# Performance work log

Hardware: AMD Instinct MI355X
Metric: run time of the kernel (lower is better)

The kernel has to match this reference:

```python
import jax, jax.numpy as jnp
import numpy as np

N, C, H, O = 100000, 128, 256, 1
T, K = 8192, 32
NHEAD, DH, FF = 8, 16, 512
NEG = -1e9

def _ln(x, g, b):
    mu = x.mean(-1, keepdims=True)
    v = x.var(-1, keepdims=True)
    return (x - mu) / jnp.sqrt(v + 1e-5) * g + b


def setup_inputs() -> dict:
    key = jax.random.key(0)
    ks = jax.random.split(key, 40)
    w = lambda k, s: jax.random.normal(k, s, jnp.float32) * 0.02
    inp = {
        'x': jax.random.normal(ks[0], (N, C), jnp.float32),
        'tar_ei': jax.random.randint(ks[1], (2, T), 0, N),
        'cn_cols': jax.random.randint(ks[2], (T, K), 0, N),
        'cn_counts': jax.random.randint(ks[3], (T,), 0, K + 1),
        'beta': jnp.ones((1,), jnp.float32),
        # cn_tokenlin: Linear(4C -> C) + ReLU
        'tok_w': w(ks[4], (C, 4 * C)), 'tok_b': w(ks[5], (C,)),
        # transformer encoder layer (norm_first, nhead=8, ff=512, gelu)
        'ln1_g': jnp.ones((C,), jnp.float32), 'ln1_b': jnp.zeros((C,), jnp.float32),
        'qkv_w': w(ks[6], (3 * C, C)), 'qkv_b': w(ks[7], (3 * C,)),
        'out_w': w(ks[8], (C, C)), 'out_b': w(ks[9], (C,)),
        'ln2_g': jnp.ones((C,), jnp.float32), 'ln2_b': jnp.zeros((C,), jnp.float32),
        'ff1_w': w(ks[10], (FF, C)), 'ff1_b': w(ks[11], (FF,)),
        'ff2_w': w(ks[12], (C, FF)), 'ff2_b': w(ks[13], (C,)),
        # xcnlin: Linear(C,H) ReLU Linear(H,H) ReLU Linear(H,H)
        'xcn_w1': w(ks[14], (H, C)), 'xcn_b1': w(ks[15], (H,)),
        'xcn_w2': w(ks[16], (H, H)), 'xcn_b2': w(ks[17], (H,)),
        'xcn_w3': w(ks[18], (H, H)), 'xcn_b3': w(ks[19], (H,)),
        # xijlin: Linear(C,H) ReLU Linear(H,H)
        'xij_w1': w(ks[20], (H, C)), 'xij_b1': w(ks[21], (H,)),
        'xij_w2': w(ks[22], (H, H)), 'xij_b2': w(ks[23], (H,)),
        # lin: Linear(H,H) ReLU Linear(H,O)
        'lin_w1': w(ks[24], (H, H)), 'lin_b1': w(ks[25], (H,)),
        'lin_w2': w(ks[26], (O, H)), 'lin_b2': w(ks[27], (O,)),
    }
    return inp


def _forward(x, beta, tok_w, tok_b, ln1_g, ln1_b, qkv_w, qkv_b, out_w, out_b,
             ln2_g, ln2_b, ff1_w, ff1_b, ff2_w, ff2_b,
             xcn_w1, xcn_b1, xcn_w2, xcn_b2, xcn_w3, xcn_b3,
             xij_w1, xij_b1, xij_w2, xij_b2, lin_w1, lin_b1, lin_w2, lin_b2,
             tar_ei, cn_cols, cn_counts):
    xi = x[tar_ei[0]]              # [T,C]
    xj = x[tar_ei[1]]              # [T,C]
    mask = jnp.arange(K)[None, :] < cn_counts[:, None]   # [T,K] valid token mask

    # --- per-(edge, common-neighbor) token features -----------------------
    xw = x[cn_cols]                # [T,K,C] gather of CN node features
    bc = lambda a: jnp.broadcast_to(a[:, None, :], (T, K, C))
    pf = jnp.concatenate([xw, bc(xi), bc(xj), bc(xi * xj)], axis=-1)  # [T,K,4C]
    tok = jax.nn.relu(pf @ tok_w.T + tok_b)               # [T,K,C]

    # --- pre-norm transformer encoder layer over the CN tokens ------------
    h = _ln(tok, ln1_g, ln1_b)
    qkv = h @ qkv_w.T + qkv_b
    q, k, v = jnp.split(qkv, 3, axis=-1)
    q = q.reshape(T, K, NHEAD, DH)
    k = k.reshape(T, K, NHEAD, DH)
    v = v.reshape(T, K, NHEAD, DH)
    scores = jnp.einsum('tqhd,tkhd->thqk', q, k) / jnp.sqrt(jnp.float32(DH))
    scores = jnp.where(mask[:, None, None, :], scores, NEG)  # key_padding_mask
    attn = jax.nn.softmax(scores, axis=-1)
    ctx = jnp.einsum('thqk,tkhd->tqhd', attn, v).reshape(T, K, C)
    tok = tok + ctx @ out_w.T + out_b
    h2 = _ln(tok, ln2_g, ln2_b)
    tok = tok + jax.nn.gelu(h2 @ ff1_w.T + ff1_b, approximate=False) @ ff2_w.T + ff2_b

    # mask out padding, mean-pool over valid CN tokens ----------------------
    tok = jnp.where(mask[..., None], tok, 0.0)
    denom = jnp.clip(cn_counts, 1)[:, None].astype(tok.dtype)
    xcn = tok.sum(axis=1) / denom                           # [T,C]; zero rows for 0 CNs

    # --- edge MLPs ---------------------------------------------------------
    hc = jax.nn.relu(xcn @ xcn_w1.T + xcn_b1)
    hc = jax.nn.relu(hc @ xcn_w2.T + xcn_b2)
    hc = hc @ xcn_w3.T + xcn_b3                              # xcnlin(xcn)
    xij = jax.nn.relu((xi * xj) @ xij_w1.T + xij_b1)
    xij = xij @ xij_w2.T + xij_b2                            # xijlin(xi*xj)
    z = jax.nn.relu((hc * beta + xij) @ lin_w1.T + lin_b1)
    return z @ lin_w2.T + lin_b2                             # [T,O]


def reference(x, tar_ei, cn_cols, cn_counts, beta, tok_w, tok_b, ln1_g, ln1_b,
              qkv_w, qkv_b, out_w, out_b, ln2_g, ln2_b, ff1_w, ff1_b, ff2_w, ff2_b,
              xcn_w1, xcn_b1, xcn_w2, xcn_b2, xcn_w3, xcn_b3,
              xij_w1, xij_b1, xij_w2, xij_b2, lin_w1, lin_b1, lin_w2, lin_b2):
    return _forward(x, beta, tok_w, tok_b, ln1_g, ln1_b, qkv_w, qkv_b, out_w, out_b,
                    ln2_g, ln2_b, ff1_w, ff1_b, ff2_w, ff2_b,
                    xcn_w1, xcn_b1, xcn_w2, xcn_b2, xcn_w3, xcn_b3,
                    xij_w1, xij_b1, xij_w2, xij_b2, lin_w1, lin_b1, lin_w2, lin_b2,
                    tar_ei, cn_cols, cn_counts)
```

## Files before the change

kernel.cpp:

```cpp
#include <hip/hip_runtime.h>
#include <hip/hip_bf16.h>
#include <math.h>

#define DI __device__ __forceinline__

typedef float  f32x4 __attribute__((ext_vector_type(4)));
typedef short  bf8   __attribute__((ext_vector_type(8)));
typedef unsigned short u16;

static constexpr int TT = 8192;
static constexpr int KK = 32;
static constexpr int CC = 128;

DI u16 f2bf(float x){ union{float f; unsigned u;} v; v.f = x; unsigned r = v.u + 0x7FFFu + ((v.u>>16)&1u); return (u16)(r>>16); }
DI float bf2f(u16 b){ union{unsigned u; float f;} v; v.u = ((unsigned)b)<<16; return v.f; }
DI unsigned pk2(float a, float b){ return (unsigned)f2bf(a) | ((unsigned)f2bf(b)<<16); }
DI f32x4 mfma16(bf8 a, bf8 b, f32x4 c){ return __builtin_amdgcn_mfma_f32_16x16x32_bf16(a, b, c, 0, 0, 0); }
DI int soff(int r, int c, int stride, int mask){ return r*stride + ((c*2) ^ ((r&mask)<<4)); }

struct WP { const float* p[12]; };

__global__ void k0_convert(WP wp, u16* __restrict__ dst){
  const int KS[11]  = {512,128,128,128,512,128,256,256,128,256,256};
  const int SH[11]  = {4,2,2,2,4,2,3,3,2,3,3};
  const int OFF[12] = {0,65536,114688,131072,196608,262144,294912,360448,425984,458752,524288,589824};
  int gid = blockIdx.x*256 + threadIdx.x;
  if (gid >= 590080) return;
  if (gid >= 589824){ dst[gid] = f2bf(wp.p[11][gid - 589824]); return; }
  #pragma unroll
  for (int s = 0; s < 11; s++){
    if (gid < OFF[s+1]){
      int i = gid - OFF[s];
      int e = i & 7, l = (i >> 3) & 63, t = i >> 9;
      int k32 = t & ((1 << SH[s]) - 1), n16 = t >> SH[s];
      int row = n16*16 + (l & 15);
      int col = k32*32 + ((l >> 4) << 3) + e;
      dst[gid] = f2bf(wp.p[s][row*KS[s] + col]);
      return;
    }
  }
}

#define O_TOK 0
#define O_H   16384
#define O_RG  32768
#define LDS_K1 53248

DI void layernorm64(const char* src, char* dst, const float* __restrict__ g,
                    const float* __restrict__ bta, int tid){
  int r = tid >> 2, q = tid & 3;
  float v[32]; float s = 0.f, sq = 0.f;
  #pragma unroll
  for (int i = 0; i < 4; i++){
    bf8 h8 = *(const bf8*)(src + soff(r, q*32 + i*8, 256, 7));
    #pragma unroll
    for (int j = 0; j < 8; j++){ float f = bf2f((u16)h8[j]); v[i*8+j] = f; s += f; sq += f*f; }
  }
  s  += __shfl_xor(s, 1);  s  += __shfl_xor(s, 2);
  sq += __shfl_xor(sq, 1); sq += __shfl_xor(sq, 2);
  float mu = s * (1.f/128.f);
  float rstd = rsqrtf(sq*(1.f/128.f) - mu*mu + 1e-5f);
  #pragma unroll
  for (int i = 0; i < 4; i++){
    bf8 o;
    #pragma unroll
    for (int j = 0; j < 8; j++){
      int c = q*32 + i*8 + j;
      o[j] = (short)f2bf((v[i*8+j] - mu)*rstd*g[c] + bta[c]);
    }
    *(bf8*)(dst + soff(r, q*32 + i*8, 256, 7)) = o;
  }
}

DI void gemm64(const char* sA, const u16* __restrict__ W, int kt, int k0t,
               int w, int l, int l15, int lg, f32x4 (&acc)[4][2]){
  #pragma unroll
  for (int ks = 0; ks < 4; ks++){
    bf8 b0 = *(const bf8*)(W + (((2*w+0)*kt + k0t + ks)*64 + l)*8);
    bf8 b1 = *(const bf8*)(W + (((2*w+1)*kt + k0t + ks)*64 + l)*8);
    #pragma unroll
    for (int mt = 0; mt < 4; mt++){
      bf8 a = *(const bf8*)(sA + soff(mt*16 + l15, ks*32 + lg*8, 256, 7));
      acc[mt][0] = mfma16(a, b0, acc[mt][0]);
      acc[mt][1] = mfma16(a, b1, acc[mt][1]);
    }
  }
}

__global__ __launch_bounds__(256, 3)
void k1_fused(const float* __restrict__ x, const int* __restrict__ tar_ei,
              const int* __restrict__ cn_cols, const int* __restrict__ cn_counts,
              const float* __restrict__ tok_b,
              const float* __restrict__ ln1_g, const float* __restrict__ ln1_b,
              const float* __restrict__ qkv_b, const float* __restrict__ out_b,
              const float* __restrict__ ln2_g, const float* __restrict__ ln2_b,
              const float* __restrict__ ff1_b, const float* __restrict__ ff2_b,
              const u16* __restrict__ wbf,
              float* __restrict__ xcn_out, float* __restrict__ xij_out)
{
  __shared__ __align__(16) char sm[LDS_K1];
  const int tid = threadIdx.x;
  const int w = tid >> 6, l = tid & 63, l15 = l & 15, lg = l >> 4;
  const int t0 = blockIdx.x * 2;

  const u16* wtok = wbf;
  const u16* wqkv = wbf + 65536;
  const u16* wout = wbf + 114688;
  const u16* wff1 = wbf + 131072;
  const u16* wff2 = wbf + 196608;

  const f32x4 zf = {0.f, 0.f, 0.f, 0.f};
  const int cnt0 = cn_counts[t0], cnt1 = cn_counts[t0 + 1];

  {
    int r = tid >> 2, q = tid & 3;
    int col = cn_cols[(t0 + (r >> 5))*KK + (r & 31)];
    const float4* xs = (const float4*)(x + (size_t)col*CC) + q*8;
    #pragma unroll
    for (int i = 0; i < 4; i++){
      float4 a = xs[2*i], b = xs[2*i+1];
      bf8 v;
      v[0]=(short)f2bf(a.x); v[1]=(short)f2bf(a.y); v[2]=(short)f2bf(a.z); v[3]=(short)f2bf(a.w);
      v[4]=(short)f2bf(b.x); v[5]=(short)f2bf(b.y); v[6]=(short)f2bf(b.z); v[7]=(short)f2bf(b.w);
      *(bf8*)(sm + O_H + soff(r, q*32 + i*8, 256, 7)) = v;
    }
  }
  if (w < 2){
    int e = w, c0 = l*2;
    int ti = tar_ei[t0 + e], tj = tar_ei[TT + t0 + e];
    float vix = x[(size_t)ti*CC + c0], viy = x[(size_t)ti*CC + c0 + 1];
    float vjx = x[(size_t)tj*CC + c0], vjy = x[(size_t)tj*CC + c0 + 1];
    float px = vix*vjx, py = viy*vjy;
    xij_out[(size_t)(t0+e)*CC + c0]     = px;
    xij_out[(size_t)(t0+e)*CC + c0 + 1] = py;
    unsigned* xb = (unsigned*)(sm + O_RG + 512) + e*192;
    xb[l]       = pk2(vix, viy);
    xb[64 + l]  = pk2(vjx, vjy);
    xb[128 + l] = pk2(px, py);
  }
  __syncthreads();

  {
    f32x4 acc[4][2];
    #pragma unroll
    for (int mt = 0; mt < 4; mt++){ acc[mt][0] = zf; acc[mt][1] = zf; }
    gemm64(sm + O_H, wtok, 16, 0, w, l, l15, lg, acc);
    #pragma unroll
    for (int c = 1; c < 4; c++){
      #pragma unroll
      for (int ks = 0; ks < 4; ks++){
        bf8 b0 = *(const bf8*)(wtok + (((2*w+0)*16 + c*4 + ks)*64 + l)*8);
        bf8 b1 = *(const bf8*)(wtok + (((2*w+1)*16 + c*4 + ks)*64 + l)*8);
        #pragma unroll
        for (int mt = 0; mt < 4; mt++){
          int e = mt >> 1;
          bf8 a = *(const bf8*)(sm + O_RG + 512 + (e*192 + (c-1)*64)*4 + (ks*32 + lg*8)*2);
          acc[mt][0] = mfma16(a, b0, acc[mt][0]);
          acc[mt][1] = mfma16(a, b1, acc[mt][1]);
        }
      }
    }
    #pragma unroll
    for (int mt = 0; mt < 4; mt++){
      #pragma unroll
      for (int nt = 0; nt < 2; nt++){
        int colg = (2*w + nt)*16 + l15;
        float tb = tok_b[colg];
        #pragma unroll
        for (int r = 0; r < 4; r++){
          int rowg = mt*16 + lg*4 + r;
          float v = fmaxf(acc[mt][nt][r] + tb, 0.f);
          *(u16*)(sm + O_TOK + soff(rowg, colg, 256, 7)) = f2bf(v);
        }
      }
    }
  }
  __syncthreads();

  layernorm64(sm + O_TOK, sm + O_H, ln1_g, ln1_b, tid);
  __syncthreads();

  unsigned pk[4][4];
  const int e_w = w >> 1, hh_w = w & 1;
  const int cnt_e = (e_w == 0) ? cnt0 : cnt1;
  char* const sQ  = sm + O_RG;
  char* const sK  = sm + O_RG + 4096;
  char* const sVT = sm + O_RG + 8192;
  char* const sAT = sm + O_RG + 12288 + w*2048;
  #pragma unroll
  for (int hc2 = 0; hc2 < 4; hc2++){
    for (int tt = w; tt < 6; tt += 4){
      int kind = tt >> 1, sub = tt & 1;
      int n16 = kind*8 + hc2*2 + sub;
      f32x4 acc[4];
      #pragma unroll
      for (int mt = 0; mt < 4; mt++) acc[mt] = zf;
      #pragma unroll
      for (int ks = 0; ks < 4; ks++){
        bf8 b = *(const bf8*)(wqkv + ((n16*4 + ks)*64 + l)*8);
        #pragma unroll
        for (int mt = 0; mt < 4; mt++){
          bf8 a = *(const bf8*)(sm + O_H + soff(mt*16 + l15, ks*32 + lg*8, 256, 7));
          acc[mt] = mfma16(a, b, acc[mt]);
        }
      }
      float bias = qkv_b[n16*16 + l15];
      #pragma unroll
      for (int mt = 0; mt < 4; mt++){
        #pragma unroll
        for (int r = 0; r < 4; r++){
          int rowg = mt*16 + lg*4 + r;
          u16 hv = f2bf(acc[mt][r] + bias);
          if (kind == 0)      *(u16*)(sQ  + soff(rowg, sub*16 + l15, 64, 3)) = hv;
          else if (kind == 1) *(u16*)(sK  + soff(rowg, sub*16 + l15, 64, 3)) = hv;
          else                *(u16*)(sVT + soff(sub*16 + l15, rowg, 128, 7)) = hv;
        }
      }
    }
    __syncthreads();

    {
      bf8 z8 = {0,0,0,0,0,0,0,0};
      bf8 qa[2], kb[2];
      #pragma unroll
      for (int mt = 0; mt < 2; mt++)
        qa[mt] = (lg < 2) ? *(const bf8*)(sQ + soff(e_w*32 + mt*16 + l15, hh_w*16 + lg*8, 64, 3)) : z8;
      #pragma unroll
      for (int nt = 0; nt < 2; nt++)
        kb[nt] = (lg < 2) ? *(const bf8*)(sK + soff(e_w*32 + nt*16 + l15, hh_w*16 + lg*8, 64, 3)) : z8;
      f32x4 sc[2][2];
      #pragma unroll
      for (int mt = 0; mt < 2; mt++)
        #pragma unroll
        for (int nt = 0; nt < 2; nt++)
          sc[mt][nt] = mfma16(qa[mt], kb[nt], zf);
      float pr[2][2][4];
      #pragma unroll
      for (int mt = 0; mt < 2; mt++)
        #pragma unroll
        for (int nt = 0; nt < 2; nt++)
          #pragma unroll
          for (int r = 0; r < 4; r++)
            pr[mt][nt][r] = (nt*16 + l15 < cnt_e) ? sc[mt][nt][r]*0.25f : -1e9f;
      #pragma unroll
      for (int mt = 0; mt < 2; mt++)
        #pragma unroll
        for (int r = 0; r < 4; r++){
          float m = fmaxf(pr[mt][0][r], pr[mt][1][r]);
          m = fmaxf(m, __shfl_xor(m, 1)); m = fmaxf(m, __shfl_xor(m, 2));
          m = fmaxf(m, __shfl_xor(m, 4)); m = fmaxf(m, __shfl_xor(m, 8));
          float e0 = __expf(pr[mt][0][r] - m), e1 = __expf(pr[mt][1][r] - m);
          float ss = e0 + e1;
          ss += __shfl_xor(ss, 1); ss += __shfl_xor(ss, 2);
          ss += __shfl_xor(ss, 4); ss += __shfl_xor(ss, 8);
          float inv = 1.f / ss;
          int rowl = mt*16 + lg*4 + r;
          *(u16*)(sAT + soff(rowl, l15,      64, 3)) = f2bf(e0*inv);
          *(u16*)(sAT + soff(rowl, 16 + l15, 64, 3)) = f2bf(e1*inv);
        }
      bf8 vb = *(const bf8*)(sVT + soff(hh_w*16 + l15, e_w*32 + lg*8, 128, 7));
      #pragma unroll
      for (int mtp = 0; mtp < 2; mtp++){
        bf8 pa = *(const bf8*)(sAT + soff(mtp*16 + l15, lg*8, 64, 3));
        f32x4 cx = mfma16(pa, vb, zf);
        pk[hc2][mtp*2+0] = pk2(cx[0], cx[1]);
        pk[hc2][mtp*2+1] = pk2(cx[2], cx[3]);
      }
    }
    __syncthreads();
  }

  #pragma unroll
  for (int hc = 0; hc < 4; hc++){
    int head = hc*2 + hh_w;
    #pragma unroll
    for (int mtp = 0; mtp < 2; mtp++)
      #pragma unroll
      for (int i = 0; i < 2; i++){
        unsigned pv = pk[hc][mtp*2+i];
        int rowg = e_w*32 + mtp*16 + lg*4 + i*2;
        *(u16*)(sm + O_RG + soff(rowg,     head*16 + l15, 256, 7)) = (u16)(pv & 0xffffu);
        *(u16*)(sm + O_RG + soff(rowg + 1, head*16 + l15, 256, 7)) = (u16)(pv >> 16);
      }
  }
  __syncthreads();

  {
    f32x4 acc[4][2];
    #pragma unroll
    for (int mt = 0; mt < 4; mt++){ acc[mt][0] = zf; acc[mt][1] = zf; }
    gemm64(sm + O_RG, wout, 4, 0, w, l, l15, lg, acc);
    #pragma unroll
    for (int mt = 0; mt < 4; mt++){
      #pragma unroll
      for (int nt = 0; nt < 2; nt++){
        int colg = (2*w + nt)*16 + l15;
        float ob = out_b[colg];
        #pragma unroll
        for (int r = 0; r < 4; r++){
          int rowg = mt*16 + lg*4 + r;
          u16* tp = (u16*)(sm + O_TOK + soff(rowg, colg, 256, 7));
          float v = acc[mt][nt][r] + ob + bf2f(*tp);
          *tp = f2bf(v);
        }
      }
    }
  }
  __syncthreads();

  layernorm64(sm + O_TOK, sm + O_H, ln2_g, ln2_b, tid);
  __syncthreads();

  f32x4 acc2[4][2];
  #pragma unroll
  for (int mt = 0; mt < 4; mt++){ acc2[mt][0] = zf; acc2[mt][1] = zf; }
  for (int c = 0; c < 4; c++){
    f32x4 acc1[4][2];
    #pragma unroll
    for (int mt = 0; mt < 4; mt++){ acc1[mt][0] = zf; acc1[mt][1] = zf; }
    gemm64(sm + O_H, wff1 + (size_t)(c*128)*128, 4, 0, w, l, l15, lg, acc1);
    #pragma unroll
    for (int mt = 0; mt < 4; mt++){
      #pragma unroll
      for (int nt = 0; nt < 2; nt++){
        int colg = (2*w + nt)*16 + l15;
        float fb = ff1_b[c*128 + colg];
        #pragma unroll
        for (int r = 0; r < 4; r++){
          int rowg = mt*16 + lg*4 + r;
          float vv = acc1[mt][nt][r] + fb;
          vv = 0.5f*vv*(1.f + erff(vv*0.70710678118654752f));
          *(u16*)(sm + O_RG + soff(rowg, colg, 256, 7)) = f2bf(vv);
        }
      }
    }
    __syncthreads();
    gemm64(sm + O_RG, wff2, 16, c*4, w, l, l15, lg, acc2);
    __syncthreads();
  }

  {
    float pool[2][2] = {};
    #pragma unroll
    for (int mt = 0; mt < 4; mt++){
      int e = mt >> 1;
      int cnt_m = (e == 0) ? cnt0 : cnt1;
      #pragma unroll
      for (int nt = 0; nt < 2; nt++){
        int colg = (2*w + nt)*16 + l15;
        float fb = ff2_b[colg];
        #pragma unroll
        for (int r = 0; r < 4; r++){
          int rowg = mt*16 + lg*4 + r;
          float tp = bf2f(*(u16*)(sm + O_TOK + soff(rowg, colg, 256, 7)));
          float v = acc2[mt][nt][r] + fb + tp;
          if ((rowg & 31) < cnt_m) pool[e][nt] += v;
        }
      }
    }
    #pragma unroll
    for (int e = 0; e < 2; e++){
      #pragma unroll
      for (int nt = 0; nt < 2; nt++){
        float v = pool[e][nt];
        v += __shfl_xor(v, 16);
        v += __shfl_xor(v, 32);
        if (lg == 0){
          int cn = (e == 0) ? cnt0 : cnt1;
          float denom = (float)(cn > 0 ? cn : 1);
          xcn_out[(size_t)(t0 + e)*CC + 32*w + nt*16 + l15] = v / denom;
        }
      }
    }
  }
}

DI void gemm32(const char* sA, int astride, int ktiles, const u16* __restrict__ W,
               int w, int l, int l15, int lg, f32x4 (&acc)[2][4]){
  for (int ks = 0; ks < ktiles; ks++){
    bf8 a0 = *(const bf8*)(sA + soff(0*16 + l15, ks*32 + lg*8, astride, 7));
    bf8 a1 = *(const bf8*)(sA + soff(1*16 + l15, ks*32 + lg*8, astride, 7));
    #pragma unroll
    for (int nt = 0; nt < 4; nt++){
      bf8 b = *(const bf8*)(W + ((((4*w+nt)*ktiles + ks))*64 + l)*8);
      acc[0][nt] = mfma16(a0, b, acc[0][nt]);
      acc[1][nt] = mfma16(a1, b, acc[1][nt]);
    }
  }
}

DI void store_h(char* dst, f32x4 (&acc)[2][4], const float* __restrict__ bias, bool relu,
                int w, int l15, int lg){
  #pragma unroll
  for (int mt = 0; mt < 2; mt++)
    #pragma unroll
    for (int nt = 0; nt < 4; nt++){
      int colg = (4*w + nt)*16 + l15;
      float bb = bias[colg];
      #pragma unroll
      for (int r = 0; r < 4; r++){
        int rowg = mt*16 + lg*4 + r;
        float v = acc[mt][nt][r] + bb;
        if (relu) v = fmaxf(v, 0.f);
        *(u16*)(dst + soff(rowg, colg, 512, 7)) = f2bf(v);
      }
    }
}

__global__ __launch_bounds__(256, 3)
void k2_mlp(const float* __restrict__ xcn, const float* __restrict__ xij,
            const u16* __restrict__ wbf,
            const float* __restrict__ xcn_b1, const float* __restrict__ xcn_b2,
            const float* __restrict__ xcn_b3, const float* __restrict__ xij_b1,
            const float* __restrict__ xij_b2, const float* __restrict__ lin_b1,
            const float* __restrict__ lin_w2, const float* __restrict__ lin_b2,
            const float* __restrict__ beta_p, float* __restrict__ out)
{
  __shared__ __align__(16) char sm[49152];
  const int O_A = 0, O_X = 8192, O_B1 = 16384, O_B2 = 32768;
  const u16* w1  = wbf + 262144;
  const u16* w2  = wbf + 294912;
  const u16* w3  = wbf + 360448;
  const u16* xw1 = wbf + 425984;
  const u16* xw2 = wbf + 458752;
  const u16* lw1 = wbf + 524288;
  const int tid = threadIdx.x;
  const int w = tid >> 6, l = tid & 63, l15 = l & 15, lg = (tid & 63) >> 4;
  const int t0 = blockIdx.x * 32;
  const f32x4 zf = {0.f,0.f,0.f,0.f};

  {
    int r = tid >> 3, ci0 = (tid & 7) * 16;
    const float4* ps = (const float4*)(xcn + (size_t)(t0 + r)*CC + ci0);
    const float4* qs = (const float4*)(xij + (size_t)(t0 + r)*CC + ci0);
    #pragma unroll
    for (int h = 0; h < 2; h++){
      float4 a = ps[2*h], b = ps[2*h+1];
      bf8 v;
      v[0]=(short)f2bf(a.x); v[1]=(short)f2bf(a.y); v[2]=(short)f2bf(a.z); v[3]=(short)f2bf(a.w);
      v[4]=(short)f2bf(b.x); v[5]=(short)f2bf(b.y); v[6]=(short)f2bf(b.z); v[7]=(short)f2bf(b.w);
      *(bf8*)(sm + O_A + soff(r, ci0 + h*8, 256, 7)) = v;
      float4 cq = qs[2*h], dq = qs[2*h+1];
      bf8 u;
      u[0]=(short)f2bf(cq.x); u[1]=(short)f2bf(cq.y); u[2]=(short)f2bf(cq.z); u[3]=(short)f2bf(cq.w);
      u[4]=(short)f2bf(dq.x); u[5]=(short)f2bf(dq.y); u[6]=(short)f2bf(dq.z); u[7]=(short)f2bf(dq.w);
      *(bf8*)(sm + O_X + soff(r, ci0 + h*8, 256, 7)) = u;
    }
  }
  __syncthreads();

  f32x4 acc[2][4];
  #pragma unroll
  for (int mt=0;mt<2;mt++) for (int nt=0;nt<4;nt++) acc[mt][nt] = zf;
  gemm32(sm + O_A, 256, 4, w1, w, l, l15, lg, acc);
  store_h(sm + O_B1, acc, xcn_b1, true, w, l15, lg);
  __syncthreads();
  #pragma unroll
  for (int mt=0;mt<2;mt++) for (int nt=0;nt<4;nt++) acc[mt][nt] = zf;
  gemm32(sm + O_B1, 512, 8, w2, w, l, l15, lg, acc);
  store_h(sm + O_B2, acc, xcn_b2, true, w, l15, lg);
  __syncthreads();
  f32x4 hc[2][4];
  #pragma unroll
  for (int mt=0;mt<2;mt++) for (int nt=0;nt<4;nt++) hc[mt][nt] = zf;
  gemm32(sm + O_B2, 512, 8, w3, w, l, l15, lg, hc);
  #pragma unroll
  for (int mt=0;mt<2;mt++) for (int nt=0;nt<4;nt++) acc[mt][nt] = zf;
  gemm32(sm + O_X, 256, 4, xw1, w, l, l15, lg, acc);
  store_h(sm + O_B1, acc, xij_b1, true, w, l15, lg);
  __syncthreads();
  f32x4 x2[2][4];
  #pragma unroll
  for (int mt=0;mt<2;mt++) for (int nt=0;nt<4;nt++) x2[mt][nt] = zf;
  gemm32(sm + O_B1, 512, 8, xw2, w, l, l15, lg, x2);
  {
    float beta = beta_p[0];
    #pragma unroll
    for (int mt = 0; mt < 2; mt++)
      #pragma unroll
      for (int nt = 0; nt < 4; nt++){
        int colg = (4*w + nt)*16 + l15;
        float b3v = xcn_b3[colg], xbv = xij_b2[colg];
        #pragma unroll
        for (int r = 0; r < 4; r++){
          int rowg = mt*16 + lg*4 + r;
          float v = (hc[mt][nt][r] + b3v)*beta + (x2[mt][nt][r] + xbv);
          *(u16*)(sm + O_B2 + soff(rowg, colg, 512, 7)) = f2bf(v);
        }
      }
  }
  __syncthreads();
  #pragma unroll
  for (int mt=0;mt<2;mt++) for (int nt=0;nt<4;nt++) acc[mt][nt] = zf;
  gemm32(sm + O_B2, 512, 8, lw1, w, l, l15, lg, acc);
  store_h(sm + O_B1, acc, lin_b1, true, w, l15, lg);
  __syncthreads();
  {
    int e = tid >> 3, li = tid & 7;
    float s = 0.f;
    #pragma unroll
    for (int i = 0; i < 32; i++){
      int c = li*32 + i;
      s += bf2f(*(u16*)(sm + O_B1 + soff(e, c, 512, 7))) * lin_w2[c];
    }
    s += __shfl_xor(s, 1); s += __shfl_xor(s, 2); s += __shfl_xor(s, 4);
    if (li == 0) out[t0 + e] = s + lin_b2[0];
  }
}

extern "C" void kernel_launch(void* const* d_in, const int* in_sizes, int n_in,
                              void* d_out, int out_size, void* d_ws, size_t ws_size,
                              hipStream_t stream){
  (void)in_sizes; (void)n_in; (void)out_size; (void)ws_size;
  const float* x        = (const float*)d_in[0];
  const int*   tar_ei   = (const int*)  d_in[1];
  const int*   cn_cols  = (const int*)  d_in[2];
  const int*   cn_cnt   = (const int*)  d_in[3];
  const float* beta     = (const float*)d_in[4];
  const float* tok_w    = (const float*)d_in[5];
  const float* tok_b    = (const float*)d_in[6];
  const float* ln1_g    = (const float*)d_in[7];
  const float* ln1_b    = (const float*)d_in[8];
  const float* qkv_w    = (const float*)d_in[9];
  const float* qkv_b    = (const float*)d_in[10];
  const float* out_w    = (const float*)d_in[11];
  const float* out_b    = (const float*)d_in[12];
  const float* ln2_g    = (const float*)d_in[13];
  const float* ln2_b    = (const float*)d_in[14];
  const float* ff1_w    = (const float*)d_in[15];
  const float* ff1_b    = (const float*)d_in[16];
  const float* ff2_w    = (const float*)d_in[17];
  const float* ff2_b    = (const float*)d_in[18];
  const float* xcn_w1   = (const float*)d_in[19];
  const float* xcn_b1   = (const float*)d_in[20];
  const float* xcn_w2   = (const float*)d_in[21];
  const float* xcn_b2   = (const float*)d_in[22];
  const float* xcn_w3   = (const float*)d_in[23];
  const float* xcn_b3   = (const float*)d_in[24];
  const float* xij_w1   = (const float*)d_in[25];
  const float* xij_b1   = (const float*)d_in[26];
  const float* xij_w2   = (const float*)d_in[27];
  const float* xij_b2   = (const float*)d_in[28];
  const float* lin_w1   = (const float*)d_in[29];
  const float* lin_b1   = (const float*)d_in[30];
  const float* lin_w2   = (const float*)d_in[31];
  const float* lin_b2   = (const float*)d_in[32];

  u16*   wbf = (u16*)d_ws;
  float* xcn = (float*)((char*)d_ws + (size_t)(2u<<20));
  float* xij = (float*)((char*)d_ws + (size_t)(6u<<20));

  WP wp;
  wp.p[0]=tok_w; wp.p[1]=qkv_w; wp.p[2]=out_w; wp.p[3]=ff1_w; wp.p[4]=ff2_w;
  wp.p[5]=xcn_w1; wp.p[6]=xcn_w2; wp.p[7]=xcn_w3; wp.p[8]=xij_w1; wp.p[9]=xij_w2;
  wp.p[10]=lin_w1; wp.p[11]=lin_w2;

  k0_convert<<<dim3(2305), dim3(256), 0, stream>>>(wp, wbf);
  k1_fused<<<dim3(TT/2), dim3(256), 0, stream>>>(
      x, tar_ei, cn_cols, cn_cnt, tok_b, ln1_g, ln1_b, qkv_b, out_b,
      ln2_g, ln2_b, ff1_b, ff2_b, wbf, xcn, xij);
  k2_mlp<<<dim3(TT/32), dim3(256), 0, stream>>>(
      xcn, xij, wbf, xcn_b1, xcn_b2, xcn_b3, xij_b1, xij_b2,
      lin_b1, lin_w2, lin_b2, beta, (float*)d_out);
}
```

Before: 613.9 us.

## Repartition k1 GEMMs by row per wave and halve k2 tile size

In the fused transformer kernel, each wave now owns 16 rows across all output columns instead of a column slice across all 64 rows. Attention is computed per wave in private LDS buffers for its edge and four heads, and the FF1/FF2 chain runs per wave through private GELU buffers. Together these remove most block-wide __syncthreads barriers. The MLP kernel processes 16 edges per block with less LDS and a higher occupancy hint. In exchange, each wave re-reads every weight tile from global/L2, so weight traffic per block goes up, and the k2 grid doubles.

```diff
diff --git a/kernel.cpp b/kernel.cpp
--- a/kernel.cpp
+++ b/kernel.cpp
@@ -69,21 +69,6 @@
       o[j] = (short)f2bf((v[i*8+j] - mu)*rstd*g[c] + bta[c]);
     }
     *(bf8*)(dst + soff(r, q*32 + i*8, 256, 7)) = o;
-  }
-}
-
-DI void gemm64(const char* sA, const u16* __restrict__ W, int kt, int k0t,
-               int w, int l, int l15, int lg, f32x4 (&acc)[4][2]){
-  #pragma unroll
-  for (int ks = 0; ks < 4; ks++){
-    bf8 b0 = *(const bf8*)(W + (((2*w+0)*kt + k0t + ks)*64 + l)*8);
-    bf8 b1 = *(const bf8*)(W + (((2*w+1)*kt + k0t + ks)*64 + l)*8);
-    #pragma unroll
-    for (int mt = 0; mt < 4; mt++){
-      bf8 a = *(const bf8*)(sA + soff(mt*16 + l15, ks*32 + lg*8, 256, 7));
-      acc[mt][0] = mfma16(a, b0, acc[mt][0]);
-      acc[mt][1] = mfma16(a, b1, acc[mt][1]);
-    }
   }
 }
 
@@ -102,6 +87,7 @@
   const int tid = threadIdx.x;
   const int w = tid >> 6, l = tid & 63, l15 = l & 15, lg = l >> 4;
   const int t0 = blockIdx.x * 2;
+  const int e_w = w >> 1, hh_w = w & 1;
 
   const u16* wtok = wbf;
   const u16* wqkv = wbf + 65536;
@@ -110,7 +96,7 @@
   const u16* wff2 = wbf + 196608;
 
   const f32x4 zf = {0.f, 0.f, 0.f, 0.f};
-  const int cnt0 = cn_counts[t0], cnt1 = cn_counts[t0 + 1];
+  const int cnt_e = cn_counts[t0 + e_w];
 
   {
     int r = tid >> 2, q = tid & 3;
@@ -141,143 +127,135 @@
   __syncthreads();
 
   {
-    f32x4 acc[4][2];
-    #pragma unroll
-    for (int mt = 0; mt < 4; mt++){ acc[mt][0] = zf; acc[mt][1] = zf; }
-    gemm64(sm + O_H, wtok, 16, 0, w, l, l15, lg, acc);
+    f32x4 acc[8];
+    #pragma unroll
+    for (int nt = 0; nt < 8; nt++) acc[nt] = zf;
+    #pragma unroll
+    for (int ks = 0; ks < 4; ks++){
+      bf8 a = *(const bf8*)(sm + O_H + soff(w*16 + l15, ks*32 + lg*8, 256, 7));
+      #pragma unroll
+      for (int nt = 0; nt < 8; nt++){
+        bf8 b = *(const bf8*)(wtok + ((nt*16 + ks)*64 + l)*8);
+        acc[nt] = mfma16(a, b, acc[nt]);
+      }
+    }
     #pragma unroll
     for (int c = 1; c < 4; c++){
       #pragma unroll
       for (int ks = 0; ks < 4; ks++){
-        bf8 b0 = *(const bf8*)(wtok + (((2*w+0)*16 + c*4 + ks)*64 + l)*8);
-        bf8 b1 = *(const bf8*)(wtok + (((2*w+1)*16 + c*4 + ks)*64 + l)*8);
+        bf8 a = *(const bf8*)(sm + O_RG + 512 + (e_w*192 + (c-1)*64)*4 + (ks*32 + lg*8)*2);
         #pragma unroll
-        for (int mt = 0; mt < 4; mt++){
-          int e = mt >> 1;
-          bf8 a = *(const bf8*)(sm + O_RG + 512 + (e*192 + (c-1)*64)*4 + (ks*32 + lg*8)*2);
-          acc[mt][0] = mfma16(a, b0, acc[mt][0]);
-          acc[mt][1] = mfma16(a, b1, acc[mt][1]);
+        for (int nt = 0; nt < 8; nt++){
+          bf8 b = *(const bf8*)(wtok + ((nt*16 + c*4 + ks)*64 + l)*8);
+          acc[nt] = mfma16(a, b, acc[nt]);
         }
       }
     }
     #pragma unroll
-    for (int mt = 0; mt < 4; mt++){
-      #pragma unroll
-      for (int nt = 0; nt < 2; nt++){
-        int colg = (2*w + nt)*16 + l15;
-        float tb = tok_b[colg];
+    for (int nt = 0; nt < 8; nt++){
+      int colg = nt*16 + l15;
+      float tb = tok_b[colg];
+      #pragma unroll
+      for (int r = 0; r < 4; r++){
+        int rowg = w*16 + lg*4 + r;
+        float v = fmaxf(acc[nt][r] + tb, 0.f);
+        *(u16*)(sm + O_TOK + soff(rowg, colg, 256, 7)) = f2bf(v);
+      }
+    }
+  }
+  layernorm64(sm + O_TOK, sm + O_H, ln1_g, ln1_b, tid);
+  __syncthreads();
+
+  char* const qbuf = sm + O_RG + w*5120;
+  char* const kbuf = qbuf + 1024;
+  char* const vbuf = qbuf + 2048;
+  char* const abuf = qbuf + 3072;
+  unsigned pkc[4][4];
+  #pragma unroll
+  for (int hi = 0; hi < 4; hi++){
+    const int h = hh_w*4 + hi;
+    f32x4 qa2[2] = {zf, zf}, ka2[2] = {zf, zf}, va2[2] = {zf, zf};
+    #pragma unroll
+    for (int ks = 0; ks < 4; ks++){
+      bf8 a0 = *(const bf8*)(sm + O_H + soff(e_w*32 + l15,      ks*32 + lg*8, 256, 7));
+      bf8 a1 = *(const bf8*)(sm + O_H + soff(e_w*32 + 16 + l15, ks*32 + lg*8, 256, 7));
+      bf8 bq = *(const bf8*)(wqkv + ((( 0 + h)*4 + ks)*64 + l)*8);
+      bf8 bk = *(const bf8*)(wqkv + ((( 8 + h)*4 + ks)*64 + l)*8);
+      bf8 bv = *(const bf8*)(wqkv + (((16 + h)*4 + ks)*64 + l)*8);
+      qa2[0] = mfma16(a0, bq, qa2[0]); qa2[1] = mfma16(a1, bq, qa2[1]);
+      ka2[0] = mfma16(a0, bk, ka2[0]); ka2[1] = mfma16(a1, bk, ka2[1]);
+      va2[0] = mfma16(a0, bv, va2[0]); va2[1] = mfma16(a1, bv, va2[1]);
+    }
+    float qbias = qkv_b[h*16 + l15];
+    float kbias = qkv_b[128 + h*16 + l15];
+    float vbias = qkv_b[256 + h*16 + l15];
+    #pragma unroll
+    for (int mt = 0; mt < 2; mt++){
+      #pragma unroll
+      for (int r = 0; r < 4; r++){
+        int row = mt*16 + lg*4 + r;
+        *(u16*)(qbuf + row*32 + l15*2) = f2bf(qa2[mt][r] + qbias);
+        *(u16*)(kbuf + row*32 + l15*2) = f2bf(ka2[mt][r] + kbias);
+        *(u16*)(vbuf + l15*64 + row*2) = f2bf(va2[mt][r] + vbias);
+      }
+    }
+    bf8 z8 = {0,0,0,0,0,0,0,0};
+    bf8 qa[2], kf[2];
+    #pragma unroll
+    for (int mt = 0; mt < 2; mt++)
+      qa[mt] = (lg < 2) ? *(const bf8*)(qbuf + (mt*16 + l15)*32 + lg*16) : z8;
+    #pragma unroll
+    for (int nt = 0; nt < 2; nt++)
+      kf[nt] = (lg < 2) ? *(const bf8*)(kbuf + (nt*16 + l15)*32 + lg*16) : z8;
+    f32x4 sc[2][2];
+    #pragma unroll
+    for (int mt = 0; mt < 2; mt++)
+      #pragma unroll
+      for (int nt = 0; nt < 2; nt++)
+        sc[mt][nt] = mfma16(qa[mt], kf[nt], zf);
+    float pr[2][2][4];
+    #pragma unroll
+    for (int mt = 0; mt < 2; mt++)
+      #pragma unroll
+      for (int nt = 0; nt < 2; nt++)
         #pragma unroll
-        for (int r = 0; r < 4; r++){
-          int rowg = mt*16 + lg*4 + r;
-          float v = fmaxf(acc[mt][nt][r] + tb, 0.f);
-          *(u16*)(sm + O_TOK + soff(rowg, colg, 256, 7)) = f2bf(v);
-        }
-      }
-    }
-  }
-  __syncthreads();
-
-  layernorm64(sm + O_TOK, sm + O_H, ln1_g, ln1_b, tid);
-  __syncthreads();
-
-  unsigned pk[4][4];
-  const int e_w = w >> 1, hh_w = w & 1;
-  const int cnt_e = (e_w == 0) ? cnt0 : cnt1;
-  char* const sQ  = sm + O_RG;
-  char* const sK  = sm + O_RG + 4096;
-  char* const sVT = sm + O_RG + 8192;
-  char* const sAT = sm + O_RG + 12288 + w*2048;
-  #pragma unroll
-  for (int hc2 = 0; hc2 < 4; hc2++){
-    for (int tt = w; tt < 6; tt += 4){
-      int kind = tt >> 1, sub = tt & 1;
-      int n16 = kind*8 + hc2*2 + sub;
-      f32x4 acc[4];
-      #pragma unroll
-      for (int mt = 0; mt < 4; mt++) acc[mt] = zf;
-      #pragma unroll
-      for (int ks = 0; ks < 4; ks++){
-        bf8 b = *(const bf8*)(wqkv + ((n16*4 + ks)*64 + l)*8);
-        #pragma unroll
-        for (int mt = 0; mt < 4; mt++){
-          bf8 a = *(const bf8*)(sm + O_H + soff(mt*16 + l15, ks*32 + lg*8, 256, 7));
-          acc[mt] = mfma16(a, b, acc[mt]);
-        }
-      }
-      float bias = qkv_b[n16*16 + l15];
-      #pragma unroll
-      for (int mt = 0; mt < 4; mt++){
-        #pragma unroll
-        for (int r = 0; r < 4; r++){
-          int rowg = mt*16 + lg*4 + r;
-          u16 hv = f2bf(acc[mt][r] + bias);
-          if (kind == 0)      *(u16*)(sQ  + soff(rowg, sub*16 + l15, 64, 3)) = hv;
-          else if (kind == 1) *(u16*)(sK  + soff(rowg, sub*16 + l15, 64, 3)) = hv;
-          else                *(u16*)(sVT + soff(sub*16 + l15, rowg, 128, 7)) = hv;
-        }
-      }
-    }
-    __syncthreads();
-
-    {
-      bf8 z8 = {0,0,0,0,0,0,0,0};
-      bf8 qa[2], kb[2];
-      #pragma unroll
-      for (int mt = 0; mt < 2; mt++)
-        qa[mt] = (lg < 2) ? *(const bf8*)(sQ + soff(e_w*32 + mt*16 + l15, hh_w*16 + lg*8, 64, 3)) : z8;
-      #pragma unroll
-      for (int nt = 0; nt < 2; nt++)
-        kb[nt] = (lg < 2) ? *(const bf8*)(sK + soff(e_w*32 + nt*16 + l15, hh_w*16 + lg*8, 64, 3)) : z8;
-      f32x4 sc[2][2];
-      #pragma unroll
-      for (int mt = 0; mt < 2; mt++)
-        #pragma unroll
-        for (int nt = 0; nt < 2; nt++)
-          sc[mt][nt] = mfma16(qa[mt], kb[nt], zf);
-      float pr[2][2][4];
-      #pragma unroll
-      for (int mt = 0; mt < 2; mt++)
-        #pragma unroll
-        for (int nt = 0; nt < 2; nt++)
-          #pragma unroll
-          for (int r = 0; r < 4; r++)
-            pr[mt][nt][r] = (nt*16 + l15 < cnt_e) ? sc[mt][nt][r]*0.25f : -1e9f;
-      #pragma unroll
-      for (int mt = 0; mt < 2; mt++)
-        #pragma unroll
-        for (int r = 0; r < 4; r++){
-          float m = fmaxf(pr[mt][0][r], pr[mt][1][r]);
-          m = fmaxf(m, __shfl_xor(m, 1)); m = fmaxf(m, __shfl_xor(m, 2));
-          m = fmaxf(m, __shfl_xor(m, 4)); m = fmaxf(m, __shfl_xor(m, 8));
-          float e0 = __expf(pr[mt][0][r] - m), e1 = __expf(pr[mt][1][r] - m);
-          float ss = e0 + e1;
-          ss += __shfl_xor(ss, 1); ss += __shfl_xor(ss, 2);
-          ss += __shfl_xor(ss, 4); ss += __shfl_xor(ss, 8);
-          float inv = 1.f / ss;
-          int rowl = mt*16 + lg*4 + r;
-          *(u16*)(sAT + soff(rowl, l15,      64, 3)) = f2bf(e0*inv);
-          *(u16*)(sAT + soff(rowl, 16 + l15, 64, 3)) = f2bf(e1*inv);
-        }
-      bf8 vb = *(const bf8*)(sVT + soff(hh_w*16 + l15, e_w*32 + lg*8, 128, 7));
-      #pragma unroll
-      for (int mtp = 0; mtp < 2; mtp++){
-        bf8 pa = *(const bf8*)(sAT + soff(mtp*16 + l15, lg*8, 64, 3));
-        f32x4 cx = mfma16(pa, vb, zf);
-        pk[hc2][mtp*2+0] = pk2(cx[0], cx[1]);
-        pk[hc2][mtp*2+1] = pk2(cx[2], cx[3]);
-      }
-    }
-    __syncthreads();
-  }
-
-  #pragma unroll
-  for (int hc = 0; hc < 4; hc++){
-    int head = hc*2 + hh_w;
+        for (int r = 0; r < 4; r++)
+          pr[mt][nt][r] = (nt*16 + l15 < cnt_e) ? sc[mt][nt][r]*0.25f : -1e9f;
+    #pragma unroll
+    for (int mt = 0; mt < 2; mt++)
+      #pragma unroll
+      for (int r = 0; r < 4; r++){
+        float m = fmaxf(pr[mt][0][r], pr[mt][1][r]);
+        m = fmaxf(m, __shfl_xor(m, 1)); m = fmaxf(m, __shfl_xor(m, 2));
+        m = fmaxf(m, __shfl_xor(m, 4)); m = fmaxf(m, __shfl_xor(m, 8));
+        float e0 = __expf(pr[mt][0][r] - m), e1 = __expf(pr[mt][1][r] - m);
+        float ss = e0 + e1;
+        ss += __shfl_xor(ss, 1); ss += __shfl_xor(ss, 2);
+        ss += __shfl_xor(ss, 4); ss += __shfl_xor(ss, 8);
+        float inv = 1.f / ss;
+        int rowl = mt*16 + lg*4 + r;
+        *(u16*)(abuf + rowl*64 + l15*2)      = f2bf(e0*inv);
+        *(u16*)(abuf + rowl*64 + 32 + l15*2) = f2bf(e1*inv);
+      }
+    bf8 vb = *(const bf8*)(vbuf + l15*64 + lg*16);
+    #pragma unroll
+    for (int mtp = 0; mtp < 2; mtp++){
+      bf8 pa = *(const bf8*)(abuf + (mtp*16 + l15)*64 + lg*16);
+      f32x4 cx = mfma16(pa, vb, zf);
+      pkc[hi][mtp*2+0] = pk2(cx[0], cx[1]);
+      pkc[hi][mtp*2+1] = pk2(cx[2], cx[3]);
+    }
+  }
+  __syncthreads();
+
+  #pragma unroll
+  for (int hi = 0; hi < 4; hi++){
+    int head = hh_w*4 + hi;
     #pragma unroll
     for (int mtp = 0; mtp < 2; mtp++)
       #pragma unroll
       for (int i = 0; i < 2; i++){
-        unsigned pv = pk[hc][mtp*2+i];
+        unsigned pv = pkc[hi][mtp*2+i];
         int rowg = e_w*32 + mtp*16 + lg*4 + i*2;
         *(u16*)(sm + O_RG + soff(rowg,     head*16 + l15, 256, 7)) = (u16)(pv & 0xffffu);
         *(u16*)(sm + O_RG + soff(rowg + 1, head*16 + l15, 256, 7)) = (u16)(pv >> 16);
@@ -286,128 +264,136 @@
   __syncthreads();
 
   {
-    f32x4 acc[4][2];
-    #pragma unroll
-    for (int mt = 0; mt < 4; mt++){ acc[mt][0] = zf; acc[mt][1] = zf; }
-    gemm64(sm + O_RG, wout, 4, 0, w, l, l15, lg, acc);
-    #pragma unroll
-    for (int mt = 0; mt < 4; mt++){
-      #pragma unroll
-      for (int nt = 0; nt < 2; nt++){
-        int colg = (2*w + nt)*16 + l15;
-        float ob = out_b[colg];
-        #pragma unroll
-        for (int r = 0; r < 4; r++){
-          int rowg = mt*16 + lg*4 + r;
-          u16* tp = (u16*)(sm + O_TOK + soff(rowg, colg, 256, 7));
-          float v = acc[mt][nt][r] + ob + bf2f(*tp);
-          *tp = f2bf(v);
-        }
-      }
-    }
-  }
-  __syncthreads();
-
+    f32x4 acc[8];
+    #pragma unroll
+    for (int nt = 0; nt < 8; nt++) acc[nt] = zf;
+    #pragma unroll
+    for (int ks = 0; ks < 4; ks++){
+      bf8 a = *(const bf8*)(sm + O_RG + soff(w*16 + l15, ks*32 + lg*8, 256, 7));
+      #pragma unroll
+      for (int nt = 0; nt < 8; nt++){
+        bf8 b = *(const bf8*)(wout + ((nt*4 + ks)*64 + l)*8);
+        acc[nt] = mfma16(a, b, acc[nt]);
+      }
+    }
+    #pragma unroll
+    for (int nt = 0; nt < 8; nt++){
+      int colg = nt*16 + l15;
+      float ob = out_b[colg];
+      #pragma unroll
+      for (int r = 0; r < 4; r++){
+        int rowg = w*16 + lg*4 + r;
+        u16* tp = (u16*)(sm + O_TOK + soff(rowg, colg, 256, 7));
+        float v = acc[nt][r] + ob + bf2f(*tp);
+        *tp = f2bf(v);
+      }
+    }
+  }
   layernorm64(sm + O_TOK, sm + O_H, ln2_g, ln2_b, tid);
-  __syncthreads();
-
-  f32x4 acc2[4][2];
-  #pragma unroll
-  for (int mt = 0; mt < 4; mt++){ acc2[mt][0] = zf; acc2[mt][1] = zf; }
+
+  char* const gb = sm + O_RG + w*4096;
+  f32x4 acc2[8];
+  #pragma unroll
+  for (int nt = 0; nt < 8; nt++) acc2[nt] = zf;
+  #pragma unroll
   for (int c = 0; c < 4; c++){
-    f32x4 acc1[4][2];
-    #pragma unroll
-    for (int mt = 0; mt < 4; mt++){ acc1[mt][0] = zf; acc1[mt][1] = zf; }
-    gemm64(sm + O_H, wff1 + (size_t)(c*128)*128, 4, 0, w, l, l15, lg, acc1);
-    #pragma unroll
-    for (int mt = 0; mt < 4; mt++){
-      #pragma unroll
-      for (int nt = 0; nt < 2; nt++){
-        int colg = (2*w + nt)*16 + l15;
-        float fb = ff1_b[c*128 + colg];
-        #pragma unroll
-        for (int r = 0; r < 4; r++){
-          int rowg = mt*16 + lg*4 + r;
-          float vv = acc1[mt][nt][r] + fb;
-          vv = 0.5f*vv*(1.f + erff(vv*0.70710678118654752f));
-          *(u16*)(sm + O_RG + soff(rowg, colg, 256, 7)) = f2bf(vv);
-        }
-      }
-    }
-    __syncthreads();
-    gemm64(sm + O_RG, wff2, 16, c*4, w, l, l15, lg, acc2);
-    __syncthreads();
-  }
-
-  {
-    float pool[2][2] = {};
-    #pragma unroll
-    for (int mt = 0; mt < 4; mt++){
-      int e = mt >> 1;
-      int cnt_m = (e == 0) ? cnt0 : cnt1;
-      #pragma unroll
-      for (int nt = 0; nt < 2; nt++){
-        int colg = (2*w + nt)*16 + l15;
-        float fb = ff2_b[colg];
-        #pragma unroll
-        for (int r = 0; r < 4; r++){
-          int rowg = mt*16 + lg*4 + r;
-          float tp = bf2f(*(u16*)(sm + O_TOK + soff(rowg, colg, 256, 7)));
-          float v = acc2[mt][nt][r] + fb + tp;
-          if ((rowg & 31) < cnt_m) pool[e][nt] += v;
-        }
-      }
-    }
-    #pragma unroll
-    for (int e = 0; e < 2; e++){
-      #pragma unroll
-      for (int nt = 0; nt < 2; nt++){
-        float v = pool[e][nt];
-        v += __shfl_xor(v, 16);
-        v += __shfl_xor(v, 32);
-        if (lg == 0){
-          int cn = (e == 0) ? cnt0 : cnt1;
-          float denom = (float)(cn > 0 ? cn : 1);
-          xcn_out[(size_t)(t0 + e)*CC + 32*w + nt*16 + l15] = v / denom;
-        }
-      }
-    }
-  }
-}
-
-DI void gemm32(const char* sA, int astride, int ktiles, const u16* __restrict__ W,
-               int w, int l, int l15, int lg, f32x4 (&acc)[2][4]){
+    f32x4 acc1[8];
+    #pragma unroll
+    for (int nt = 0; nt < 8; nt++) acc1[nt] = zf;
+    #pragma unroll
+    for (int ks = 0; ks < 4; ks++){
+      bf8 a = *(const bf8*)(sm + O_H + soff(w*16 + l15, ks*32 + lg*8, 256, 7));
+      #pragma unroll
+      for (int nt = 0; nt < 8; nt++){
+        bf8 b = *(const bf8*)(wff1 + (((c*8 + nt)*4 + ks)*64 + l)*8);
+        acc1[nt] = mfma16(a, b, acc1[nt]);
+      }
+    }
+    #pragma unroll
+    for (int nt = 0; nt < 8; nt++){
+      float fb = ff1_b[c*128 + nt*16 + l15];
+      #pragma unroll
+      for (int r = 0; r < 4; r++){
+        float vv = acc1[nt][r] + fb;
+        vv = 0.5f*vv*(1.f + erff(vv*0.70710678118654752f));
+        *(u16*)(gb + soff(lg*4 + r, nt*16 + l15, 256, 7)) = f2bf(vv);
+      }
+    }
+    #pragma unroll
+    for (int ks = 0; ks < 4; ks++){
+      bf8 a = *(const bf8*)(gb + soff(l15, ks*32 + lg*8, 256, 7));
+      #pragma unroll
+      for (int nt = 0; nt < 8; nt++){
+        bf8 b = *(const bf8*)(wff2 + ((nt*16 + c*4 + ks)*64 + l)*8);
+        acc2[nt] = mfma16(a, b, acc2[nt]);
+      }
+    }
+  }
+
+  {
+    float p[8];
+    #pragma unroll
+    for (int nt = 0; nt < 8; nt++){
+      int colg = nt*16 + l15;
+      float fb = ff2_b[colg];
+      float s = 0.f;
+      #pragma unroll
+      for (int r = 0; r < 4; r++){
+        int rowg = w*16 + lg*4 + r;
+        float tp = bf2f(*(u16*)(sm + O_TOK + soff(rowg, colg, 256, 7)));
+        float v = acc2[nt][r] + fb + tp;
+        if ((rowg & 31) < cnt_e) s += v;
+      }
+      p[nt] = s;
+    }
+    float* pbuf = (float*)(sm + O_TOK + w*4096);
+    #pragma unroll
+    for (int nt = 0; nt < 8; nt++){
+      float s = p[nt];
+      s += __shfl_xor(s, 16);
+      s += __shfl_xor(s, 32);
+      if (lg == 0) pbuf[nt*16 + l15] = s;
+    }
+  }
+  __syncthreads();
+  {
+    int e = tid >> 7, col = tid & 127;
+    float s = *(const float*)(sm + O_TOK + (e*2)*4096   + col*4)
+            + *(const float*)(sm + O_TOK + (e*2+1)*4096 + col*4);
+    int cn = cn_counts[t0 + e];
+    float denom = (float)(cn > 0 ? cn : 1);
+    xcn_out[(size_t)(t0 + e)*CC + col] = s / denom;
+  }
+}
+
+DI void gemm16(const char* sA, int astride, int ktiles, const u16* __restrict__ W,
+               int w, int l, int l15, int lg, f32x4 (&acc)[4]){
   for (int ks = 0; ks < ktiles; ks++){
-    bf8 a0 = *(const bf8*)(sA + soff(0*16 + l15, ks*32 + lg*8, astride, 7));
-    bf8 a1 = *(const bf8*)(sA + soff(1*16 + l15, ks*32 + lg*8, astride, 7));
-    #pragma unroll
-    for (int nt = 0; nt < 4; nt++){
-      bf8 b = *(const bf8*)(W + ((((4*w+nt)*ktiles + ks))*64 + l)*8);
-      acc[0][nt] = mfma16(a0, b, acc[0][nt]);
-      acc[1][nt] = mfma16(a1, b, acc[1][nt]);
-    }
-  }
-}
-
-DI void store_h(char* dst, f32x4 (&acc)[2][4], const float* __restrict__ bias, bool relu,
+    bf8 a = *(const bf8*)(sA + soff(l15, ks*32 + lg*8, astride, 7));
+    #pragma unroll
+    for (int j = 0; j < 4; j++){
+      bf8 b = *(const bf8*)(W + (((4*w + j)*ktiles + ks)*64 + l)*8);
+      acc[j] = mfma16(a, b, acc[j]);
+    }
+  }
+}
+
+DI void store16(char* dst, f32x4 (&acc)[4], const float* __restrict__ bias, bool relu,
                 int w, int l15, int lg){
   #pragma unroll
-  for (int mt = 0; mt < 2; mt++)
-    #pragma unroll
-    for (int nt = 0; nt < 4; nt++){
-      int colg = (4*w + nt)*16 + l15;
-      float bb = bias[colg];
-      #pragma unroll
-      for (int r = 0; r < 4; r++){
-        int rowg = mt*16 + lg*4 + r;
-        float v = acc[mt][nt][r] + bb;
-        if (relu) v = fmaxf(v, 0.f);
-        *(u16*)(dst + soff(rowg, colg, 512, 7)) = f2bf(v);
-      }
-    }
-}
-
-__global__ __launch_bounds__(256, 3)
+  for (int j = 0; j < 4; j++){
+    int colg = (4*w + j)*16 + l15;
+    float bb = bias[colg];
+    #pragma unroll
+    for (int r = 0; r < 4; r++){
+      float v = acc[j][r] + bb;
+      if (relu) v = fmaxf(v, 0.f);
+      *(u16*)(dst + soff(lg*4 + r, colg, 512, 7)) = f2bf(v);
+    }
+  }
+}
+
+__global__ __launch_bounds__(256, 6)
 void k2_mlp(const float* __restrict__ xcn, const float* __restrict__ xij,
             const u16* __restrict__ wbf,
             const float* __restrict__ xcn_b1, const float* __restrict__ xcn_b2,
@@ -416,8 +402,8 @@
             const float* __restrict__ lin_w2, const float* __restrict__ lin_b2,
             const float* __restrict__ beta_p, float* __restrict__ out)
 {
-  __shared__ __align__(16) char sm[49152];
-  const int O_A = 0, O_X = 8192, O_B1 = 16384, O_B2 = 32768;
+  __shared__ __align__(16) char sm[24576];
+  const int O_A = 0, O_X = 4096, O_B1 = 8192, O_B2 = 16384;
   const u16* w1  = wbf + 262144;
   const u16* w2  = wbf + 294912;
   const u16* w3  = wbf + 360448;
@@ -426,84 +412,79 @@
   const u16* lw1 = wbf + 524288;
   const int tid = threadIdx.x;
   const int w = tid >> 6, l = tid & 63, l15 = l & 15, lg = (tid & 63) >> 4;
-  const int t0 = blockIdx.x * 32;
+  const int t0 = blockIdx.x * 16;
   const f32x4 zf = {0.f,0.f,0.f,0.f};
 
   {
-    int r = tid >> 3, ci0 = (tid & 7) * 16;
+    int r = tid >> 4, ci0 = (tid & 15) * 8;
     const float4* ps = (const float4*)(xcn + (size_t)(t0 + r)*CC + ci0);
     const float4* qs = (const float4*)(xij + (size_t)(t0 + r)*CC + ci0);
-    #pragma unroll
-    for (int h = 0; h < 2; h++){
-      float4 a = ps[2*h], b = ps[2*h+1];
-      bf8 v;
-      v[0]=(short)f2bf(a.x); v[1]=(short)f2bf(a.y); v[2]=(short)f2bf(a.z); v[3]=(short)f2bf(a.w);
-      v[4]=(short)f2bf(b.x); v[5]=(short)f2bf(b.y); v[6]=(short)f2bf(b.z); v[7]=(short)f2bf(b.w);
-      *(bf8*)(sm + O_A + soff(r, ci0 + h*8, 256, 7)) = v;
-      float4 cq = qs[2*h], dq = qs[2*h+1];
-      bf8 u;
-      u[0]=(short)f2bf(cq.x); u[1]=(short)f2bf(cq.y); u[2]=(short)f2bf(cq.z); u[3]=(short)f2bf(cq.w);
-      u[4]=(short)f2bf(dq.x); u[5]=(short)f2bf(dq.y); u[6]=(short)f2bf(dq.z); u[7]=(short)f2bf(dq.w);
-      *(bf8*)(sm + O_X + soff(r, ci0 + h*8, 256, 7)) = u;
-    }
-  }
-  __syncthreads();
-
-  f32x4 acc[2][4];
-  #pragma unroll
-  for (int mt=0;mt<2;mt++) for (int nt=0;nt<4;nt++) acc[mt][nt] = zf;
-  gemm32(sm + O_A, 256, 4, w1, w, l, l15, lg, acc);
-  store_h(sm + O_B1, acc, xcn_b1, true, w, l15, lg);
-  __syncthreads();
-  #pragma unroll
-  for (int mt=0;mt<2;mt++) for (int nt=0;nt<4;nt++) acc[mt][nt] = zf;
-  gemm32(sm + O_B1, 512, 8, w2, w, l, l15, lg, acc);
-  store_h(sm + O_B2, acc, xcn_b2, true, w, l15, lg);
-  __syncthreads();
-  f32x4 hc[2][4];
-  #pragma unroll
-  for (int mt=0;mt<2;mt++) for (int nt=0;nt<4;nt++) hc[mt][nt] = zf;
-  gemm32(sm + O_B2, 512, 8, w3, w, l, l15, lg, hc);
-  #pragma unroll
-  for (int mt=0;mt<2;mt++) for (int nt=0;nt<4;nt++) acc[mt][nt] = zf;
-  gemm32(sm + O_X, 256, 4, xw1, w, l, l15, lg, acc);
-  store_h(sm + O_B1, acc, xij_b1, true, w, l15, lg);
-  __syncthreads();
-  f32x4 x2[2][4];
-  #pragma unroll
-  for (int mt=0;mt<2;mt++) for (int nt=0;nt<4;nt++) x2[mt][nt] = zf;
-  gemm32(sm + O_B1, 512, 8, xw2, w, l, l15, lg, x2);
+    float4 a = ps[0], b = ps[1];
+    bf8 v;
+    v[0]=(short)f2bf(a.x); v[1]=(short)f2bf(a.y); v[2]=(short)f2bf(a.z); v[3]=(short)f2bf(a.w);
+    v[4]=(short)f2bf(b.x); v[5]=(short)f2bf(b.y); v[6]=(short)f2bf(b.z); v[7]=(short)f2bf(b.w);
+    *(bf8*)(sm + O_A + soff(r, ci0, 256, 7)) = v;
+    float4 cq = qs[0], dq = qs[1];
+    bf8 u;
+    u[0]=(short)f2bf(cq.x); u[1]=(short)f2bf(cq.y); u[2]=(short)f2bf(cq.z); u[3]=(short)f2bf(cq.w);
+    u[4]=(short)f2bf(dq.x); u[5]=(short)f2bf(dq.y); u[6]=(short)f2bf(dq.z); u[7]=(short)f2bf(dq.w);
+    *(bf8*)(sm + O_X + soff(r, ci0, 256, 7)) = u;
+  }
+  __syncthreads();
+
+  f32x4 acc[4];
+  #pragma unroll
+  for (int j=0;j<4;j++) acc[j] = zf;
+  gemm16(sm + O_A, 256, 4, w1, w, l, l15, lg, acc);
+  store16(sm + O_B1, acc, xcn_b1, true, w, l15, lg);
+  __syncthreads();
+  #pragma unroll
+  for (int j=0;j<4;j++) acc[j] = zf;
+  gemm16(sm + O_B1, 512, 8, w2, w, l, l15, lg, acc);
+  store16(sm + O_B2, acc, xcn_b2, true, w, l15, lg);
+  __syncthreads();
+  f32x4 hc[4];
+  #pragma unroll
+  for (int j=0;j<4;j++) hc[j] = zf;
+  gemm16(sm + O_B2, 512, 8, w3, w, l, l15, lg, hc);
+  #pragma unroll
+  for (int j=0;j<4;j++) acc[j] = zf;
+  gemm16(sm + O_X, 256, 4, xw1, w, l, l15, lg, acc);
+  store16(sm + O_B1, acc, xij_b1, true, w, l15, lg);
+  __syncthreads();
+  f32x4 x2[4];
+  #pragma unroll
+  for (int j=0;j<4;j++) x2[j] = zf;
+  gemm16(sm + O_B1, 512, 8, xw2, w, l, l15, lg, x2);
   {
     float beta = beta_p[0];
     #pragma unroll
-    for (int mt = 0; mt < 2; mt++)
-      #pragma unroll
-      for (int nt = 0; nt < 4; nt++){
-        int colg = (4*w + nt)*16 + l15;
-        float b3v = xcn_b3[colg], xbv = xij_b2[colg];
-        #pragma unroll
-        for (int r = 0; r < 4; r++){
-          int rowg = mt*16 + lg*4 + r;
-          float v = (hc[mt][nt][r] + b3v)*beta + (x2[mt][nt][r] + xbv);
-          *(u16*)(sm + O_B2 + soff(rowg, colg, 512, 7)) = f2bf(v);
-        }
-      }
-  }
-  __syncthreads();
-  #pragma unroll
-  for (int mt=0;mt<2;mt++) for (int nt=0;nt<4;nt++) acc[mt][nt] = zf;
-  gemm32(sm + O_B2, 512, 8, lw1, w, l, l15, lg, acc);
-  store_h(sm + O_B1, acc, lin_b1, true, w, l15, lg);
-  __syncthreads();
-  {
-    int e = tid >> 3, li = tid & 7;
+    for (int j = 0; j < 4; j++){
+      int colg = (4*w + j)*16 + l15;
+      float b3v = xcn_b3[colg], xbv = xij_b2[colg];
+      #pragma unroll
+      for (int r = 0; r < 4; r++){
+        float v = (hc[j][r] + b3v)*beta + (x2[j][r] + xbv);
+        *(u16*)(sm + O_B2 + soff(lg*4 + r, colg, 512, 7)) = f2bf(v);
+      }
+    }
+  }
+  __syncthreads();
+  #pragma unroll
+  for (int j=0;j<4;j++) acc[j] = zf;
+  gemm16(sm + O_B2, 512, 8, lw1, w, l, l15, lg, acc);
+  store16(sm + O_B1, acc, lin_b1, true, w, l15, lg);
+  __syncthreads();
+  {
+    int e = tid >> 4, li = tid & 15;
     float s = 0.f;
     #pragma unroll
-    for (int i = 0; i < 32; i++){
-      int c = li*32 + i;
+    for (int i = 0; i < 16; i++){
+      int c = li*16 + i;
       s += bf2f(*(u16*)(sm + O_B1 + soff(e, c, 512, 7))) * lin_w2[c];
     }
-    s += __shfl_xor(s, 1); s += __shfl_xor(s, 2); s += __shfl_xor(s, 4);
+    s += __shfl_xor(s, 1); s += __shfl_xor(s, 2);
+    s += __shfl_xor(s, 4); s += __shfl_xor(s, 8);
     if (li == 0) out[t0 + e] = s + lin_b2[0];
   }
 }
@@ -559,7 +540,7 @@
   k1_fused<<<dim3(TT/2), dim3(256), 0, stream>>>(
       x, tar_ei, cn_cols, cn_cnt, tok_b, ln1_g, ln1_b, qkv_b, out_b,
       ln2_g, ln2_b, ff1_b, ff2_b, wbf, xcn, xij);
-  k2_mlp<<<dim3(TT/32), dim3(256), 0, stream>>>(
+  k2_mlp<<<dim3(TT/16), dim3(256), 0, stream>>>(
       xcn, xij, wbf, xcn_b1, xcn_b2, xcn_b3, xij_b1, xij_b2,
       lin_b1, lin_w2, lin_b2, beta, (float*)d_out);
 }
```

Measured after the change: 1.007 ms. 1.64x slower.
